# Performance work log

Measured on AMD Instinct MI355X. Metric: run time of the kernel, lower is better.

## Reference

```python
import jax, jax.numpy as jnp
import numpy as np

NB_HEAD = 16

def _rope_cos_sin(pos, dim):
    # Standard RoPE frequencies, base 10000, rotate-half convention.
    inv_freq = 1.0 / (10000.0 ** (jnp.arange(0, dim, 2, dtype=jnp.float32) / dim))  # (dim/2,)
    ang = pos.astype(jnp.float32)[:, None] * inv_freq[None, :]                      # (S, dim/2)
    ang = jnp.concatenate([ang, ang], axis=-1)                                      # (S, dim)
    return jnp.cos(ang), jnp.sin(ang)

def _rotate(x, cos, sin):
    # x: (B, H, S, hd); cos/sin: (S, hd) broadcast over B, H.
    h = x.shape[-1] // 2
    x1, x2 = x[..., :h], x[..., h:]
    return x * cos + jnp.concatenate([-x2, x1], axis=-1) * sin

def setup_inputs() -> dict:
    key = jax.random.key(0)
    ks = jax.random.split(key, 8)
    B, S, D = 2, 2048, 1024
    scale = 0.02
    return {
        'query': jax.random.normal(ks[0], (B, S, D), dtype=jnp.float32),
        'key':   jax.random.normal(ks[1], (B, S, D), dtype=jnp.float32),
        'value': jax.random.normal(ks[2], (B, S, D), dtype=jnp.float32),
        'pos_enc': jnp.arange(S, dtype=jnp.int32),
        'Wk': jax.random.normal(ks[3], (D, D), dtype=jnp.float32) * scale,
        'bk': jnp.zeros((D,), dtype=jnp.float32),
        'Wv': jax.random.normal(ks[4], (D, D), dtype=jnp.float32) * scale,
        'bv': jnp.zeros((D,), dtype=jnp.float32),
        'Wo': jax.random.normal(ks[5], (D, D), dtype=jnp.float32) * scale,
        'bo': jnp.zeros((D,), dtype=jnp.float32),
    }

def reference(query, key, value, pos_enc, Wk, bk, Wv, bv, Wo, bo):
    B, S, D = query.shape
    H = NB_HEAD
    hd = D // H
    # Faithful quirk: raw reshape (B,S,D)->(B,H,S,hd), NO transpose; query unprojected.
    q = query.reshape(B, H, S, hd)
    k = (key @ Wk.T + bk).reshape(B, H, S, hd)
    v = (value @ Wv.T + bv).reshape(B, H, S, hd)
    cos, sin = _rope_cos_sin(pos_enc, hd)
    q = _rotate(q, cos, sin)
    k = _rotate(k, cos, sin)
    v = _rotate(v, cos, sin)  # RoPE applied to V as well (faithful)
    scores = jnp.einsum('bhqd,bhkd->bhqk', q, k) / jnp.sqrt(jnp.float32(hd))
    # tril(-1) + triu(1): zero the diagonal (NOT -inf masking)
    scores = scores * (1.0 - jnp.eye(S, dtype=scores.dtype))
    # softmax over dim=2 == the QUERY axis (faithful quirk)
    attn = jax.nn.softmax(scores, axis=2)
    out = jnp.einsum('bhqk,bhkd->bhqd', attn, v)     # (B,H,S,hd)
    x = out.transpose(0, 2, 1, 3).reshape(B, S, D)   # (B,S,D)
    return x @ Wo.T + bo
```

## Files before the change

### kernel.cpp

```cpp
#include <hip/hip_runtime.h>
#include <hip/hip_bf16.h>
#include <math.h>

#define B_  2
#define S_  2048
#define D_  1024
#define H_  16
#define HD_ 64
#define M_  (B_*S_)
#define BH_ (B_*H_)
#define QKSCALE 0.18033688011112042f

typedef __attribute__((ext_vector_type(8)))  short  bf16x8;
typedef __attribute__((ext_vector_type(4)))  float  f32x4;

#define MFMA16(a,b,c) __builtin_amdgcn_mfma_f32_16x16x32_bf16(a,b,c,0,0,0)

__device__ float          g_vp[(size_t)M_ * D_];
__device__ float          g_p1[(size_t)M_ * D_];
__device__ unsigned short g_q16[(size_t)M_ * D_];
__device__ unsigned short g_k16[(size_t)M_ * D_];
__device__ unsigned short g_v16t[(size_t)M_ * D_];
__device__ unsigned short g_x16[(size_t)M_ * D_];
__device__ float          g_rz[BH_ * S_];
__device__ float          g_tab[S_ * 64];

static __device__ __forceinline__ unsigned short f2b(float x){
  union { float f; unsigned u; } v; v.f = x;
  unsigned r = v.u + 0x7FFFu + ((v.u >> 16) & 1u);
  return (unsigned short)(r >> 16);
}
static __device__ __forceinline__ unsigned cvtpk(float lo, float hi){
  unsigned r;
  asm("v_cvt_pk_bf16_f32 %0, %1, %2" : "=v"(r) : "v"(lo), "v"(hi));
  return r;
}

__global__ void k_table(const int* __restrict__ pos){
  int i = blockIdx.x * 256 + threadIdx.x;
  if (i >= S_ * 32) return;
  int s = i >> 5, f = i & 31;
  float ang = (float)pos[s] * powf(10000.0f, -(float)f * (1.0f/32.0f));
  g_tab[2*i]   = cosf(ang);
  g_tab[2*i+1] = sinf(ang);
}

__global__ void k_ropeq(const float* __restrict__ in){
  const int i = blockIdx.x * 256 + threadIdx.x;
  const int grp = i >> 5, d = i & 31;
  const int s = grp & (S_ - 1);
  const size_t base = (size_t)grp * 64;
  const float x1 = in[base + d];
  const float x2 = in[base + d + 32];
  const float c  = g_tab[(s*32 + d)*2];
  const float sn = g_tab[(s*32 + d)*2 + 1];
  g_q16[base + d]      = f2b((x1*c - x2*sn) * QKSCALE);
  g_q16[base + d + 32] = f2b((x2*c + x1*sn) * QKSCALE);
}

__global__ __launch_bounds__(256) void k_proj(const float* __restrict__ key,
                                              const float* __restrict__ value,
                                              const float* __restrict__ Wk,
                                              const float* __restrict__ bk,
                                              const float* __restrict__ Wv,
                                              const float* __restrict__ bv){
  __shared__ __align__(16) unsigned short As[128*64];
  __shared__ __align__(16) unsigned short Bs[128*64];
  const int z = blockIdx.z;
  const float* A    = z ? value : key;
  const float* W    = z ? Wv : Wk;
  const float* bias = z ? bv : bk;
  const int t = threadIdx.x, l = t & 63, wid = t >> 6;
  const int wm = wid >> 1, wn = wid & 1;
  const int rowB = blockIdx.y * 128, colB = blockIdx.x * 128;
  f32x4 acc[4][4];
  #pragma unroll
  for (int i = 0; i < 4; ++i)
    #pragma unroll
    for (int j = 0; j < 4; ++j)
      #pragma unroll
      for (int r = 0; r < 4; ++r) acc[i][j][r] = 0.f;

  const int srow = t >> 3, se = (t & 7) * 8;
  float4 a0[4], a1[4], b0[4], b1[4];
#define GLD(K0) \
  for (int u = 0; u < 4; ++u){ \
    const int row = srow + u*32; \
    const float* ap = A + (size_t)(rowB+row)*D_ + (K0) + se; \
    const float* wp = W + (size_t)(colB+row)*D_ + (K0) + se; \
    a0[u] = *(const float4*)ap; a1[u] = *(const float4*)(ap+4); \
    b0[u] = *(const float4*)wp; b1[u] = *(const float4*)(wp+4); \
  }
  GLD(0);
  for (int k0 = 0; k0 < D_; k0 += 64){
    __syncthreads();
    #pragma unroll
    for (int u = 0; u < 4; ++u){
      const int row = srow + u*32;
      const int off = row*128 + ((se*2) ^ ((row & 7) << 4));
      uint4 pa, pb;
      pa.x = cvtpk(a0[u].x, a0[u].y); pa.y = cvtpk(a0[u].z, a0[u].w);
      pa.z = cvtpk(a1[u].x, a1[u].y); pa.w = cvtpk(a1[u].z, a1[u].w);
      pb.x = cvtpk(b0[u].x, b0[u].y); pb.y = cvtpk(b0[u].z, b0[u].w);
      pb.z = cvtpk(b1[u].x, b1[u].y); pb.w = cvtpk(b1[u].z, b1[u].w);
      *(uint4*)((char*)As + off) = pa;
      *(uint4*)((char*)Bs + off) = pb;
    }
    __syncthreads();
    if (k0 + 64 < D_){ GLD(k0 + 64); }
    #pragma unroll
    for (int kk = 0; kk < 2; ++kk){
      const int cb = kk*64 + (l >> 4) * 16;
      bf16x8 af[4], bfr[4];
      #pragma unroll
      for (int mi = 0; mi < 4; ++mi){
        const int row = wm*64 + mi*16 + (l & 15);
        af[mi] = *(const bf16x8*)((const char*)As + row*128 + (cb ^ ((row & 7) << 4)));
      }
      #pragma unroll
      for (int ni = 0; ni < 4; ++ni){
        const int row = wn*64 + ni*16 + (l & 15);
        bfr[ni] = *(const bf16x8*)((const char*)Bs + row*128 + (cb ^ ((row & 7) << 4)));
      }
      #pragma unroll
      for (int mi = 0; mi < 4; ++mi)
        #pragma unroll
        for (int ni = 0; ni < 4; ++ni)
          acc[mi][ni] = MFMA16(af[mi], bfr[ni], acc[mi][ni]);
    }
  }
#undef GLD
  const int ql15 = l & 15, r4 = (l >> 4) * 4;
  const int hcol = (colB >> 6) + wn;
  #pragma unroll
  for (int mi = 0; mi < 4; ++mi){
    #pragma unroll
    for (int r = 0; r < 4; ++r){
      const int row = rowB + wm*64 + mi*16 + r4 + r;
      const int pos = ((row & 127) << 4) + hcol;
      #pragma unroll
      for (int ni = 0; ni < 2; ++ni){
        const int col = colB + wn*64 + ni*16 + ql15;
        const int f = ni*16 + ql15;
        const float c  = g_tab[(pos*32 + f)*2];
        const float sn = g_tab[(pos*32 + f)*2 + 1];
        const float x1 = acc[mi][ni][r]   + bias[col];
        const float x2 = acc[mi][ni+2][r] + bias[col+32];
        const float o1 = x1*c - x2*sn;
        const float o2 = x2*c + x1*sn;
        if (z){
          g_vp[(size_t)row*D_ + col]      = o1;
          g_vp[(size_t)row*D_ + col + 32] = o2;
        } else {
          g_k16[(size_t)row*D_ + col]      = f2b(o1);
          g_k16[(size_t)row*D_ + col + 32] = f2b(o2);
        }
      }
    }
  }
}

__global__ __launch_bounds__(256) void k_gemm_out(const unsigned short* __restrict__ A,
                                                  const float* __restrict__ W,
                                                  const float* __restrict__ bias,
                                                  float* __restrict__ C){
  __shared__ __align__(16) unsigned short As[128*64];
  __shared__ __align__(16) unsigned short Bs[128*64];
  const int t = threadIdx.x, l = t & 63, wid = t >> 6;
  const int wm = wid >> 1, wn = wid & 1;
  const int rowB = blockIdx.y * 128, colB = blockIdx.x * 128;
  f32x4 acc[4][4];
  #pragma unroll
  for (int i = 0; i < 4; ++i)
    #pragma unroll
    for (int j = 0; j < 4; ++j)
      #pragma unroll
      for (int r = 0; r < 4; ++r) acc[i][j][r] = 0.f;

  const int srow = t >> 3, se = (t & 7) * 8, scb = (t & 7) * 16;
  float4 ar[4], b0[4], b1[4];
#define GLD(K0) \
  for (int u = 0; u < 4; ++u){ \
    const int row = srow + u*32; \
    ar[u] = *(const float4*)((const char*)(A + (size_t)(rowB+row)*D_ + (K0)) + scb); \
    const float* wp = W + (size_t)(colB+row)*D_ + (K0) + se; \
    b0[u] = *(const float4*)wp; b1[u] = *(const float4*)(wp+4); \
  }
  GLD(0);
  for (int k0 = 0; k0 < D_; k0 += 64){
    __syncthreads();
    #pragma unroll
    for (int u = 0; u < 4; ++u){
      const int row = srow + u*32;
      const int off = row*128 + (scb ^ ((row & 7) << 4));
      uint4 pb;
      pb.x = cvtpk(b0[u].x, b0[u].y); pb.y = cvtpk(b0[u].z, b0[u].w);
      pb.z = cvtpk(b1[u].x, b1[u].y); pb.w = cvtpk(b1[u].z, b1[u].w);
      *(float4*)((char*)As + off) = ar[u];
      *(uint4*)((char*)Bs + off) = pb;
    }
    __syncthreads();
    if (k0 + 64 < D_){ GLD(k0 + 64); }
    #pragma unroll
    for (int kk = 0; kk < 2; ++kk){
      const int cb = kk*64 + (l >> 4) * 16;
      bf16x8 af[4], bfr[4];
      #pragma unroll
      for (int mi = 0; mi < 4; ++mi){
        const int row = wm*64 + mi*16 + (l & 15);
        af[mi] = *(const bf16x8*)((const char*)As + row*128 + (cb ^ ((row & 7) << 4)));
      }
      #pragma unroll
      for (int ni = 0; ni < 4; ++ni){
        const int row = wn*64 + ni*16 + (l & 15);
        bfr[ni] = *(const bf16x8*)((const char*)Bs + row*128 + (cb ^ ((row & 7) << 4)));
      }
      #pragma unroll
      for (int mi = 0; mi < 4; ++mi)
        #pragma unroll
        for (int ni = 0; ni < 4; ++ni)
          acc[mi][ni] = MFMA16(af[mi], bfr[ni], acc[mi][ni]);
    }
  }
#undef GLD
  #pragma unroll
  for (int mi = 0; mi < 4; ++mi){
    #pragma unroll
    for (int ni = 0; ni < 4; ++ni){
      const int col = colB + wn*64 + ni*16 + (l & 15);
      const float bb = bias[col];
      #pragma unroll
      for (int r = 0; r < 4; ++r){
        const int row = rowB + wm*64 + mi*16 + (l >> 4)*4 + r;
        C[(size_t)row * D_ + col] = acc[mi][ni][r] + bb;
      }
    }
  }
}

__global__ __launch_bounds__(256) void k_pass1(){
  __shared__ float zs[4][4][16];
  const int t = threadIdx.x, l = t & 63, wid = t >> 6;
  const int bh = blockIdx.y;
  const int kwb = blockIdx.x * 64;
  const unsigned short* Qp = g_q16 + (size_t)bh * S_ * HD_;
  const unsigned short* Kp = g_k16 + (size_t)bh * S_ * HD_;
  bf16x8 bk_[4][2];
  #pragma unroll
  for (int kb = 0; kb < 4; ++kb){
    const unsigned short* kr = Kp + (size_t)(kwb + kb*16 + (l & 15)) * HD_ + (l >> 4) * 8;
    bk_[kb][0] = *(const bf16x8*)(kr);
    bk_[kb][1] = *(const bf16x8*)(kr + 32);
  }
  float zz[4] = {0.f, 0.f, 0.f, 0.f};
  const int qBeg = wid * (S_/4);
  for (int qi = 0; qi < S_/4; qi += 16){
    const int q0 = qBeg + qi;
    const unsigned short* qr = Qp + (size_t)(q0 + (l & 15)) * HD_ + (l >> 4) * 8;
    bf16x8 a0 = *(const bf16x8*)(qr);
    bf16x8 a1 = *(const bf16x8*)(qr + 32);
    #pragma unroll
    for (int kb = 0; kb < 4; ++kb){
      f32x4 c = {0.f, 0.f, 0.f, 0.f};
      c = MFMA16(a0, bk_[kb][0], c);
      c = MFMA16(a1, bk_[kb][1], c);
      if (q0 == kwb + kb*16){
        const int kg = kwb + kb*16 + (l & 15);
        #pragma unroll
        for (int r = 0; r < 4; ++r)
          zz[kb] += (q0 + (l >> 4)*4 + r == kg) ? 1.0f : exp2f(c[r]);
      } else {
        zz[kb] += exp2f(c[0]) + exp2f(c[1]) + exp2f(c[2]) + exp2f(c[3]);
      }
    }
  }
  #pragma unroll
  for (int kb = 0; kb < 4; ++kb){
    float z = zz[kb];
    z += __shfl_xor(z, 16); z += __shfl_xor(z, 32);
    if (l < 16) zs[wid][kb][l] = z;
  }
  __syncthreads();
  if (t < 64){
    const int kb = t >> 4, ki = t & 15;
    const float Z = zs[0][kb][ki] + zs[1][kb][ki] + zs[2][kb][ki] + zs[3][kb][ki];
    g_rz[bh*S_ + kwb + kb*16 + ki] = 1.0f / Z;
  }
}

__global__ __launch_bounds__(256) void k_vfix(){
  __shared__ __align__(16) float tile[64][68];
  const int t = threadIdx.x;
  const int bh = blockIdx.y;
  const int s0 = blockIdx.x * 64;
  #pragma unroll
  for (int u = 0; u < 4; ++u){
    const int i = t + u*256;
    const int row = i >> 4, c4 = (i & 15) * 4;
    *(float4*)&tile[row][c4] = *(const float4*)(g_vp + (size_t)(bh*S_ + s0 + row) * HD_ + c4);
  }
  __syncthreads();
  const int d = t >> 2;
  const int sc = (t & 3) * 16;
  float rzv[16];
  #pragma unroll
  for (int u = 0; u < 4; ++u)
    *(float4*)&rzv[u*4] = *(const float4*)(g_rz + bh*S_ + s0 + sc + u*4);
  unsigned w[8];
  #pragma unroll
  for (int j2 = 0; j2 < 8; ++j2)
    w[j2] = cvtpk(tile[sc + 2*j2][d] * rzv[2*j2], tile[sc + 2*j2 + 1][d] * rzv[2*j2 + 1]);
  unsigned short* dst = g_v16t + (size_t)(bh*HD_ + d) * S_ + s0 + sc;
  *(uint4*)(dst)     = *(uint4*)&w[0];
  *(uint4*)(dst + 8) = *(uint4*)&w[4];
}

__global__ __launch_bounds__(256, 4) void k_pass2(){
  __shared__ __align__(16) unsigned short Ks[64*64];
  __shared__ __align__(16) unsigned short Vs[64*64];
  __shared__ __align__(16) unsigned short Ps[4*32*64];
  const int t = threadIdx.x, l = t & 63, wid = t >> 6;
  const int bh = blockIdx.y;
  const int z = blockIdx.z;
  const int b = bh >> 4, hh = bh & 15;
  const int q0 = blockIdx.x * 128;
  const unsigned short* Qp = g_q16  + (size_t)bh * S_ * HD_;
  const unsigned short* Kp = g_k16  + (size_t)bh * S_ * HD_;
  const unsigned short* Vp = g_v16t + (size_t)bh * HD_ * S_;
  float* Op = z ? g_p1 : g_vp;
  const int ql = l & 15, kq = l >> 4;
  const int qb = q0 + wid*32;
  char* Pw = (char*)Ps + wid * 4096;

  bf16x8 qf[2][2];
  #pragma unroll
  for (int h = 0; h < 2; ++h){
    const unsigned short* qr = Qp + (size_t)(qb + h*16 + ql) * HD_ + kq * 8;
    qf[h][0] = *(const bf16x8*)(qr);
    qf[h][1] = *(const bf16x8*)(qr + 32);
  }
  f32x4 co[4][2];
  #pragma unroll
  for (int nd = 0; nd < 4; ++nd)
    #pragma unroll
    for (int h = 0; h < 2; ++h)
      #pragma unroll
      for (int r = 0; r < 4; ++r) co[nd][h][r] = 0.f;

  const int srow = t >> 3, scb = (t & 7) * 16;
  const int kg0 = z * (S_/2);
  float4 kreg[2], vreg[2];
  #pragma unroll
  for (int u = 0; u < 2; ++u){
    kreg[u] = *(const float4*)((const char*)(Kp + (size_t)(kg0 + srow + u*32) * HD_) + scb);
    vreg[u] = *(const float4*)((const char*)(Vp + (size_t)(srow + u*32) * S_ + kg0) + scb);
  }
  for (int kt = 0; kt < 16; ++kt){
    const int k0 = kg0 + kt * 64;
    __syncthreads();
    #pragma unroll
    for (int u = 0; u < 2; ++u){
      const int row = srow + u*32;
      const int off = row*128 + (scb ^ ((row & 7) << 4));
      *(float4*)((char*)Ks + off) = kreg[u];
      *(float4*)((char*)Vs + off) = vreg[u];
    }
    __syncthreads();
    if (kt < 15){
      const int k1 = k0 + 64;
      #pragma unroll
      for (int u = 0; u < 2; ++u){
        kreg[u] = *(const float4*)((const char*)(Kp + (size_t)(k1 + srow + u*32) * HD_) + scb);
        vreg[u] = *(const float4*)((const char*)(Vp + (size_t)(srow + u*32) * S_ + k1) + scb);
      }
    }
    f32x4 cst[4][2];
    #pragma unroll
    for (int kb = 0; kb < 4; ++kb)
      #pragma unroll
      for (int h = 0; h < 2; ++h)
        #pragma unroll
        for (int r = 0; r < 4; ++r) cst[kb][h][r] = 0.f;
    #pragma unroll
    for (int kb = 0; kb < 4; ++kb){
      const int row = kb*16 + ql;
      #pragma unroll
      for (int s = 0; s < 2; ++s){
        bf16x8 kf = *(const bf16x8*)((const char*)Ks + row*128 + ((s*64 + kq*16) ^ ((row & 7) << 4)));
        cst[kb][0] = MFMA16(kf, qf[0][s], cst[kb][0]);
        cst[kb][1] = MFMA16(kf, qf[1][s], cst[kb][1]);
      }
    }
    const bool diag = (k0 < qb + 32) && (qb < k0 + 64);
    #pragma unroll
    for (int h = 0; h < 2; ++h){
      const int qg = qb + h*16 + ql;
      #pragma unroll
      for (int kb = 0; kb < 4; ++kb){
        float e[4];
        if (diag){
          #pragma unroll
          for (int r = 0; r < 4; ++r){
            const int key = k0 + kb*16 + kq*4 + r;
            e[r] = (qg == key) ? 1.0f : exp2f(cst[kb][h][r]);
          }
        } else {
          #pragma unroll
          for (int r = 0; r < 4; ++r) e[r] = exp2f(cst[kb][h][r]);
        }
        uint2 w;
        w.x = cvtpk(e[0], e[1]);
        w.y = cvtpk(e[2], e[3]);
        *(uint2*)(Pw + (h*16 + ql)*128 + ((kb*32 + kq*8) ^ ((ql & 7) << 4))) = w;
      }
    }
    #pragma unroll
    for (int sl = 0; sl < 2; ++sl){
      bf16x8 pf0 = *(const bf16x8*)(Pw + (0*16 + ql)*128 + ((sl*64 + kq*16) ^ ((ql & 7) << 4)));
      bf16x8 pf1 = *(const bf16x8*)(Pw + (1*16 + ql)*128 + ((sl*64 + kq*16) ^ ((ql & 7) << 4)));
      #pragma unroll
      for (int nd = 0; nd < 4; ++nd){
        const int row = nd*16 + ql;
        bf16x8 vf = *(const bf16x8*)((const char*)Vs + row*128 + ((sl*64 + kq*16) ^ ((row & 7) << 4)));
        co[nd][0] = MFMA16(pf0, vf, co[nd][0]);
        co[nd][1] = MFMA16(pf1, vf, co[nd][1]);
      }
    }
  }
  #pragma unroll
  for (int h = 0; h < 2; ++h){
    #pragma unroll
    for (int nd = 0; nd < 4; ++nd){
      const int d = nd*16 + ql;
      #pragma unroll
      for (int r = 0; r < 4; ++r){
        const int q = qb + h*16 + kq*4 + r;
        Op[(size_t)(b*S_ + q) * D_ + hh*HD_ + d] = co[nd][h][r];
      }
    }
  }
}

__global__ void k_reduce(){
  const int i = blockIdx.x * 256 + threadIdx.x;
  const size_t off = (size_t)i * 8;
  float4 a0 = *(const float4*)(g_vp + off), a1 = *(const float4*)(g_vp + off + 4);
  float4 b0 = *(const float4*)(g_p1 + off), b1 = *(const float4*)(g_p1 + off + 4);
  uint4 w;
  w.x = cvtpk(a0.x + b0.x, a0.y + b0.y);
  w.y = cvtpk(a0.z + b0.z, a0.w + b0.w);
  w.z = cvtpk(a1.x + b1.x, a1.y + b1.y);
  w.w = cvtpk(a1.z + b1.z, a1.w + b1.w);
  *(uint4*)(g_x16 + off) = w;
}

extern "C" void kernel_launch(void* const* d_in, const int* in_sizes, int n_in,
                              void* d_out, int out_size, void* d_ws, size_t ws_size,
                              hipStream_t stream) {
  const float* query = (const float*)d_in[0];
  const float* key   = (const float*)d_in[1];
  const float* value = (const float*)d_in[2];
  const int*   pos   = (const int*)  d_in[3];
  const float* Wk    = (const float*)d_in[4];
  const float* bk    = (const float*)d_in[5];
  const float* Wv    = (const float*)d_in[6];
  const float* bv    = (const float*)d_in[7];
  const float* Wo    = (const float*)d_in[8];
  const float* bo    = (const float*)d_in[9];
  float* out = (float*)d_out;

  unsigned short* px16; hipGetSymbolAddress((void**)&px16, HIP_SYMBOL(g_x16));

  k_table<<<256, 256, 0, stream>>>(pos);

  dim3 gP(D_/128, M_/128, 2);
  k_proj<<<gP, 256, 0, stream>>>(key, value, Wk, bk, Wv, bv);

  k_ropeq<<<8192, 256, 0, stream>>>(query);

  k_pass1<<<dim3(S_/64, BH_), 256, 0, stream>>>();
  k_vfix <<<dim3(32, BH_), 256, 0, stream>>>();
  k_pass2<<<dim3(16, BH_, 2), 256, 0, stream>>>();
  k_reduce<<<(M_*D_/8)/256, 256, 0, stream>>>();

  dim3 gO(D_/128, M_/128);
  k_gemm_out<<<gO, 256, 0, stream>>>(px16, Wo, bo, out);
}
```

Measured before the change: 246.5 us.

## Split attention key range four ways and read K/V fragments directly from global

The PV pass now splits the key dimension into four chunks instead of two, doubling grid parallelism, and the reduce kernel sums four fp32 partials. K and V tiles are no longer staged through shared memory with block barriers; each wave loads its MFMA fragments straight from global memory, and the per-wave P buffer is double-buffered across iterations. This drops the __syncthreads and LDS staging traffic, but it adds redundant global/L2 reads of K/V across waves and two more full-size fp32 partial buffers to write and read back.

```diff
diff --git a/kernel.cpp b/kernel.cpp
--- a/kernel.cpp
+++ b/kernel.cpp
@@ -18,6 +18,8 @@
 
 __device__ float          g_vp[(size_t)M_ * D_];
 __device__ float          g_p1[(size_t)M_ * D_];
+__device__ float          g_p2[(size_t)M_ * D_];
+__device__ float          g_p3[(size_t)M_ * D_];
 __device__ unsigned short g_q16[(size_t)M_ * D_];
 __device__ unsigned short g_k16[(size_t)M_ * D_];
 __device__ unsigned short g_v16t[(size_t)M_ * D_];
@@ -316,9 +318,7 @@
 }
 
 __global__ __launch_bounds__(256, 4) void k_pass2(){
-  __shared__ __align__(16) unsigned short Ks[64*64];
-  __shared__ __align__(16) unsigned short Vs[64*64];
-  __shared__ __align__(16) unsigned short Ps[4*32*64];
+  __shared__ __align__(16) unsigned short Ps[2][4][32*64];
   const int t = threadIdx.x, l = t & 63, wid = t >> 6;
   const int bh = blockIdx.y;
   const int z = blockIdx.z;
@@ -327,10 +327,9 @@
   const unsigned short* Qp = g_q16  + (size_t)bh * S_ * HD_;
   const unsigned short* Kp = g_k16  + (size_t)bh * S_ * HD_;
   const unsigned short* Vp = g_v16t + (size_t)bh * HD_ * S_;
-  float* Op = z ? g_p1 : g_vp;
+  float* Op = (z == 0) ? g_vp : (z == 1) ? g_p1 : (z == 2) ? g_p2 : g_p3;
   const int ql = l & 15, kq = l >> 4;
   const int qb = q0 + wid*32;
-  char* Pw = (char*)Ps + wid * 4096;
 
   bf16x8 qf[2][2];
   #pragma unroll
@@ -347,33 +346,11 @@
       #pragma unroll
       for (int r = 0; r < 4; ++r) co[nd][h][r] = 0.f;
 
-  const int srow = t >> 3, scb = (t & 7) * 16;
-  const int kg0 = z * (S_/2);
-  float4 kreg[2], vreg[2];
-  #pragma unroll
-  for (int u = 0; u < 2; ++u){
-    kreg[u] = *(const float4*)((const char*)(Kp + (size_t)(kg0 + srow + u*32) * HD_) + scb);
-    vreg[u] = *(const float4*)((const char*)(Vp + (size_t)(srow + u*32) * S_ + kg0) + scb);
-  }
-  for (int kt = 0; kt < 16; ++kt){
+  const int kg0 = z * (S_/4);
+  #pragma unroll 2
+  for (int kt = 0; kt < 8; ++kt){
     const int k0 = kg0 + kt * 64;
-    __syncthreads();
-    #pragma unroll
-    for (int u = 0; u < 2; ++u){
-      const int row = srow + u*32;
-      const int off = row*128 + (scb ^ ((row & 7) << 4));
-      *(float4*)((char*)Ks + off) = kreg[u];
-      *(float4*)((char*)Vs + off) = vreg[u];
-    }
-    __syncthreads();
-    if (kt < 15){
-      const int k1 = k0 + 64;
-      #pragma unroll
-      for (int u = 0; u < 2; ++u){
-        kreg[u] = *(const float4*)((const char*)(Kp + (size_t)(k1 + srow + u*32) * HD_) + scb);
-        vreg[u] = *(const float4*)((const char*)(Vp + (size_t)(srow + u*32) * S_ + k1) + scb);
-      }
-    }
+    char* Pw = (char*)&Ps[kt & 1][wid][0];
     f32x4 cst[4][2];
     #pragma unroll
     for (int kb = 0; kb < 4; ++kb)
@@ -383,13 +360,13 @@
         for (int r = 0; r < 4; ++r) cst[kb][h][r] = 0.f;
     #pragma unroll
     for (int kb = 0; kb < 4; ++kb){
-      const int row = kb*16 + ql;
-      #pragma unroll
-      for (int s = 0; s < 2; ++s){
-        bf16x8 kf = *(const bf16x8*)((const char*)Ks + row*128 + ((s*64 + kq*16) ^ ((row & 7) << 4)));
-        cst[kb][0] = MFMA16(kf, qf[0][s], cst[kb][0]);
-        cst[kb][1] = MFMA16(kf, qf[1][s], cst[kb][1]);
-      }
+      const unsigned short* kr = Kp + (size_t)(k0 + kb*16 + ql) * HD_ + kq * 8;
+      bf16x8 kf0 = *(const bf16x8*)(kr);
+      bf16x8 kf1 = *(const bf16x8*)(kr + 32);
+      cst[kb][0] = MFMA16(kf0, qf[0][0], cst[kb][0]);
+      cst[kb][0] = MFMA16(kf1, qf[0][1], cst[kb][0]);
+      cst[kb][1] = MFMA16(kf0, qf[1][0], cst[kb][1]);
+      cst[kb][1] = MFMA16(kf1, qf[1][1], cst[kb][1]);
     }
     const bool diag = (k0 < qb + 32) && (qb < k0 + 64);
     #pragma unroll
@@ -420,8 +397,8 @@
       bf16x8 pf1 = *(const bf16x8*)(Pw + (1*16 + ql)*128 + ((sl*64 + kq*16) ^ ((ql & 7) << 4)));
       #pragma unroll
       for (int nd = 0; nd < 4; ++nd){
-        const int row = nd*16 + ql;
-        bf16x8 vf = *(const bf16x8*)((const char*)Vs + row*128 + ((sl*64 + kq*16) ^ ((row & 7) << 4)));
+        const unsigned short* vr = Vp + (size_t)(nd*16 + ql) * S_ + k0 + sl*32 + kq*8;
+        bf16x8 vf = *(const bf16x8*)(vr);
         co[nd][0] = MFMA16(pf0, vf, co[nd][0]);
         co[nd][1] = MFMA16(pf1, vf, co[nd][1]);
       }
@@ -446,11 +423,13 @@
   const size_t off = (size_t)i * 8;
   float4 a0 = *(const float4*)(g_vp + off), a1 = *(const float4*)(g_vp + off + 4);
   float4 b0 = *(const float4*)(g_p1 + off), b1 = *(const float4*)(g_p1 + off + 4);
+  float4 c0 = *(const float4*)(g_p2 + off), c1 = *(const float4*)(g_p2 + off + 4);
+  float4 d0 = *(const float4*)(g_p3 + off), d1 = *(const float4*)(g_p3 + off + 4);
   uint4 w;
-  w.x = cvtpk(a0.x + b0.x, a0.y + b0.y);
-  w.y = cvtpk(a0.z + b0.z, a0.w + b0.w);
-  w.z = cvtpk(a1.x + b1.x, a1.y + b1.y);
-  w.w = cvtpk(a1.z + b1.z, a1.w + b1.w);
+  w.x = cvtpk(a0.x + b0.x + c0.x + d0.x, a0.y + b0.y + c0.y + d0.y);
+  w.y = cvtpk(a0.z + b0.z + c0.z + d0.z, a0.w + b0.w + c0.w + d0.w);
+  w.z = cvtpk(a1.x + b1.x + c1.x + d1.x, a1.y + b1.y + c1.y + d1.y);
+  w.w = cvtpk(a1.z + b1.z + c1.z + d1.z, a1.w + b1.w + c1.w + d1.w);
   *(uint4*)(g_x16 + off) = w;
 }
 
@@ -480,7 +459,7 @@
 
   k_pass1<<<dim3(S_/64, BH_), 256, 0, stream>>>();
   k_vfix <<<dim3(32, BH_), 256, 0, stream>>>();
-  k_pass2<<<dim3(16, BH_, 2), 256, 0, stream>>>();
+  k_pass2<<<dim3(16, BH_, 4), 256, 0, stream>>>();
   k_reduce<<<(M_*D_/8)/256, 256, 0, stream>>>();
 
   dim3 gO(D_/128, M_/128);
```

After: 291.3 us. +18.2%, slower.
